# Performance work log

Hardware: AMD Instinct MI355X
Metric: run time of the kernel (lower is better)

The kernel has to match this reference:

```python
import jax, jax.numpy as jnp
import numpy as np

N = 4096       # num nodes
E = 131072     # num edges (avg degree 32)
IN = 256
HID = 512
OUT = 64


def _linear_params(k, fan_in, fan_out):
    kw, kb = jax.random.split(k)
    s = 1.0 / np.sqrt(fan_in)
    W = jax.random.uniform(kw, (fan_in, fan_out), jnp.float32, -s, s)
    b = jax.random.uniform(kb, (fan_out,), jnp.float32, -s, s)
    return W, b


def setup_inputs() -> dict:
    key = jax.random.key(0)
    ks = jax.random.split(key, 8)
    x = jax.random.normal(ks[0], (N, IN), jnp.float32)
    edge_index = jax.random.randint(ks[1], (2, E), 0, N, jnp.int32)
    ego_W, ego_b = _linear_params(ks[2], IN, HID)
    cut_W, cut_b = _linear_params(ks[3], IN, HID)
    glob_W, glob_b = _linear_params(ks[4], IN, HID)
    fc_W, fc_b = _linear_params(ks[5], 3 * HID, OUT)
    return dict(x=x, edge_index=edge_index, ego_W=ego_W, ego_b=ego_b,
                cut_W=cut_W, cut_b=cut_b, glob_W=glob_W, glob_b=glob_b,
                fc_W=fc_W, fc_b=fc_b)


def reference(x, edge_index, ego_W, ego_b, cut_W, cut_b, glob_W, glob_b, fc_W, fc_b):
    src, dst = edge_index[0], edge_index[1]
    n = x.shape[0]

    # --- extract_ego_subgraph: mean of x over the unique 2-hop in-neighborhood
    # (k_hop_subgraph flow='source_to_target': walk edges backward), incl. self.
    # B[t, s] = 1 iff edge s -> t exists.
    B = jnp.zeros((n, n), jnp.float32).at[dst, src].set(1.0)
    eye = jnp.eye(n, dtype=jnp.float32)
    reach = ((eye + B + B @ B) > 0).astype(jnp.float32)   # [N, N] bool-as-float
    ego_feat = (reach @ x) / reach.sum(axis=1, keepdims=True)  # counts >= 1 (self)

    # --- extract_cut_subgraph: drop a random half of the edges, then mean of
    # target features over kept out-edges per source node; fallback to x.
    perm = jax.random.permutation(jax.random.key(42), E)
    keep = jnp.ones(E, bool).at[perm[: E // 2]].set(False).astype(x.dtype)  # [E]
    sums = jax.ops.segment_sum(x[dst] * keep[:, None], src, num_segments=n)
    cnt = jax.ops.segment_sum(keep, src, num_segments=n)
    cut_feat = jnp.where((cnt > 0)[:, None], sums / jnp.maximum(cnt, 1.0)[:, None], x)

    # --- MessagePassingLayer: relu(scatter_add(linear(x)[src] -> dst))
    def mp(feat, W, b):
        h = feat @ W + b
        agg = jax.ops.segment_sum(h[src], dst, num_segments=n)
        return jax.nn.relu(agg)

    ego_enc = mp(ego_feat, ego_W, ego_b)
    cut_enc = mp(cut_feat, cut_W, cut_b)
    glob_enc = x @ glob_W + glob_b

    combined = jnp.concatenate([ego_enc, cut_enc, glob_enc], axis=-1)  # [N, 3H]
    out = combined @ fc_W + fc_b
    return jax.nn.log_softmax(out, axis=1)
```

## Files before the change

### kernel.cpp

```cpp
#include <hip/hip_runtime.h>

#define NN 4096
#define NE 131072
#define DIN 256
#define DHID 512
#define DOUT 64
#define DCAT 1536
#define NBINS 65536
#define HALF_E 65536

typedef __attribute__((ext_vector_type(8))) short short8;
typedef __attribute__((ext_vector_type(4))) float f32x4;

__device__ inline unsigned short bf16rne(float f){
  unsigned u = __float_as_uint(f);
  unsigned r = u + 0x7FFFu + ((u>>16)&1u);
  return (unsigned short)(r>>16);
}
__device__ inline float bf2f(unsigned short u){ return __uint_as_float(((unsigned)u)<<16); }

struct K2 { unsigned a, b; };
__host__ __device__ constexpr unsigned rotl32(unsigned x, unsigned d){ return (x<<d)|(x>>(32u-d)); }
__host__ __device__ constexpr K2 tf2x32(unsigned k0, unsigned k1, unsigned x0, unsigned x1){
  unsigned k2 = k0 ^ k1 ^ 0x1BD11BDAu;
  x0 += k0; x1 += k1;
  x0+=x1; x1=rotl32(x1,13); x1^=x0;
  x0+=x1; x1=rotl32(x1,15); x1^=x0;
  x0+=x1; x1=rotl32(x1,26); x1^=x0;
  x0+=x1; x1=rotl32(x1, 6); x1^=x0;
  x0+=k1; x1+=k2+1u;
  x0+=x1; x1=rotl32(x1,17); x1^=x0;
  x0+=x1; x1=rotl32(x1,29); x1^=x0;
  x0+=x1; x1=rotl32(x1,16); x1^=x0;
  x0+=x1; x1=rotl32(x1,24); x1^=x0;
  x0+=k2; x1+=k0+2u;
  x0+=x1; x1=rotl32(x1,13); x1^=x0;
  x0+=x1; x1=rotl32(x1,15); x1^=x0;
  x0+=x1; x1=rotl32(x1,26); x1^=x0;
  x0+=x1; x1=rotl32(x1, 6); x1^=x0;
  x0+=k0; x1+=k1+3u;
  x0+=x1; x1=rotl32(x1,17); x1^=x0;
  x0+=x1; x1=rotl32(x1,29); x1^=x0;
  x0+=x1; x1=rotl32(x1,16); x1^=x0;
  x0+=x1; x1=rotl32(x1,24); x1^=x0;
  x0+=k1; x1+=k2+4u;
  x0+=x1; x1=rotl32(x1,13); x1^=x0;
  x0+=x1; x1=rotl32(x1,15); x1^=x0;
  x0+=x1; x1=rotl32(x1,26); x1^=x0;
  x0+=x1; x1=rotl32(x1, 6); x1^=x0;
  x0+=k2; x1+=k0+5u;
  return K2{x0,x1};
}
static_assert(tf2x32(0u,0u,0u,2u).a==4146024105u, "threefry mismatch o0");
static_assert(tf2x32(0u,0u,0u,2u).b==2718843009u, "threefry mismatch o1");
static_assert(tf2x32(0u,0u,1u,3u).a==967050713u,  "threefry mismatch o0b");
static_assert(tf2x32(0u,0u,1u,3u).b==1272950319u, "threefry mismatch o1b");

constexpr K2 E0 = tf2x32(0u,42u,0u,0u);
constexpr K2 E1 = tf2x32(0u,42u,0u,1u);
constexpr unsigned SK1A = E1.a, SK1B = E1.b;
constexpr K2 F1 = tf2x32(E0.a,E0.b,0u,1u);
constexpr unsigned SK2A = F1.a, SK2B = F1.b;

#define MED_CAP 64

__device__ inline void tconv(const float* __restrict__ src, unsigned short* __restrict__ dst,
                             int R, int C, int r0, int c0){
  __shared__ unsigned short tile[64][72];
  int t = threadIdx.x;
  int tr = t>>2, tc = (t&3)*16;
  #pragma unroll
  for (int u=0;u<16;u++)
    tile[tr][tc+u] = bf16rne(src[(size_t)(r0+tr)*C + c0 + tc + u]);
  __syncthreads();
  unsigned short v[16];
  #pragma unroll
  for (int u=0;u<16;u++) v[u] = tile[tc+u][tr];
  uint4* vv = (uint4*)v;
  uint4* o = (uint4*)&dst[(size_t)(c0+tr)*R + r0 + tc];
  o[0] = vv[0]; o[1] = vv[1];
}

__global__ void front_k(const int* __restrict__ ei,
                        unsigned* __restrict__ keys1, unsigned* __restrict__ keys2,
                        unsigned* __restrict__ hist1, unsigned* __restrict__ hist2,
                        unsigned* __restrict__ indeg, unsigned* __restrict__ outdeg,
                        unsigned* __restrict__ bits,
                        const float* __restrict__ x, unsigned short* __restrict__ x_bf,
                        unsigned short* __restrict__ xT_bf,
                        const float* __restrict__ W0, unsigned short* __restrict__ WT0,
                        const float* __restrict__ W1, unsigned short* __restrict__ WT1,
                        const float* __restrict__ W2, unsigned short* __restrict__ WT2,
                        const float* __restrict__ fcW, unsigned short* __restrict__ fcWT){
  int b = blockIdx.x, t = threadIdx.x;
  if (b < 512){
    unsigned e = b*256u + t;
    K2 r1 = tf2x32(SK1A, SK1B, 0u, e);
    unsigned k1 = r1.a ^ r1.b;
    K2 r2 = tf2x32(SK2A, SK2B, 0u, e);
    unsigned k2 = r2.a ^ r2.b;
    keys1[e] = k1; keys2[e] = k2;
    atomicAdd(&hist1[k1>>16], 1u);
    atomicAdd(&hist2[k2>>16], 1u);
    unsigned s = (unsigned)ei[e], d = (unsigned)ei[NE+e];
    atomicAdd(&outdeg[s], 1u);
    atomicAdd(&indeg[d], 1u);
    atomicOr(&bits[d*128 + (s>>5)], 1u << (s&31));
    if (e < NN) atomicOr(&bits[e*128 + (e>>5)], 1u << (e&31));
    return;
  }
  int b2 = b - 512;
  if (b2 < 256){
    __shared__ unsigned short tile[64][72];
    int r0 = (b2>>2)*64, c0 = (b2&3)*64;
    int tr = t>>2, tc = (t&3)*16;
    #pragma unroll
    for (int u=0;u<16;u++)
      tile[tr][tc+u] = bf16rne(x[(size_t)(r0+tr)*DIN + c0 + tc + u]);
    __syncthreads();
    unsigned short vr[16];
    #pragma unroll
    for (int u=0;u<16;u++) vr[u] = tile[tr][tc+u];
    uint4* rv = (uint4*)vr;
    uint4* xo = (uint4*)&x_bf[(size_t)(r0+tr)*DIN + c0 + tc];
    xo[0] = rv[0]; xo[1] = rv[1];
    unsigned short v[16];
    #pragma unroll
    for (int u=0;u<16;u++) v[u] = tile[tc+u][tr];
    uint4* vv = (uint4*)v;
    uint4* o = (uint4*)&xT_bf[(size_t)(c0+tr)*NN + r0 + tc];
    o[0] = vv[0]; o[1] = vv[1];
  } else if (b2 < 352){
    int idx = b2 - 256;
    int z = idx >> 5, tl = idx & 31;
    const float* src = z==0?W0 : z==1?W1 : W2;
    unsigned short* dst = z==0?WT0 : z==1?WT1 : WT2;
    tconv(src, dst, DIN, DHID, (tl>>3)*64, (tl&7)*64);
  } else {
    int by = b2 - 352;
    tconv(fcW, fcWT, DCAT, DOUT, by*64, 0);
  }
}

__global__ void scanAll_k(const unsigned* __restrict__ in0, const unsigned* __restrict__ in1,
                          const unsigned* __restrict__ in2, const unsigned* __restrict__ in3,
                          unsigned* __restrict__ o0, unsigned* __restrict__ o1,
                          unsigned* __restrict__ o2, unsigned* __restrict__ o3,
                          unsigned* __restrict__ c0, unsigned* __restrict__ c1,
                          unsigned* __restrict__ c2, unsigned* __restrict__ c3,
                          unsigned* __restrict__ flags, const unsigned* __restrict__ hist2,
                          unsigned* __restrict__ med){
  int y = blockIdx.y;
  int nblk = (y<2) ? (NBINS/256) : (NN/256);
  int xb = blockIdx.x;
  if (xb >= nblk) return;
  const unsigned* in = y==0?in0 : y==1?in1 : y==2?in2 : in3;
  unsigned* o        = y==0?o0  : y==1?o1  : y==2?o2  : o3;
  unsigned* c        = y==0?c0  : y==1?c1  : y==2?c2  : c3;
  __shared__ unsigned s[256];
  __shared__ unsigned base_s;
  int t = threadIdx.x; unsigned i = xb*256u + t;
  unsigned v = in[i]; s[t] = v; __syncthreads();
  for (int off=1; off<256; off<<=1){
    unsigned u = (t>=off)?s[t-off]:0u; __syncthreads();
    s[t]+=u; __syncthreads();
  }
  unsigned excl = s[t]-v;
  unsigned total = s[255];
  unsigned* f = flags + y*256;
  if (xb == 0){
    if (t==0){ atomicExch(&f[0], 0x80000000u | total); base_s = 0u; }
  } else {
    if (t==0) atomicExch(&f[xb], 0x40000000u | total);
    if (t < 64){
      unsigned base = 0; int start = xb-1; int done = 0;
      while (!done && start >= 0){
        int idx = start - t;
        unsigned fv = 0;
        if (idx >= 0){
          do { fv = atomicAdd(&f[idx], 0u); } while (!(fv & 0xC0000000u));
        }
        unsigned long long pm = __ballot(idx >= 0 && (fv & 0x80000000u));
        unsigned contrib;
        if (pm){
          int plane = __ffsll((long long)pm) - 1;
          contrib = (idx >= 0 && t <= plane) ? (fv & 0x3FFFFFFFu) : 0u;
          done = 1;
        } else {
          contrib = (idx >= 0) ? (fv & 0x3FFFFFFFu) : 0u;
          start -= 64;
        }
        for (int oo=32; oo>0; oo>>=1) contrib += __shfl_xor(contrib, oo, 64);
        base += contrib;
      }
      if (t==0){ atomicExch(&f[xb], 0x80000000u | (base + total)); base_s = base; }
    }
  }
  __syncthreads();
  unsigned res = excl + base_s;
  o[i] = res; c[i] = res;
  if (y==1){
    unsigned hv = hist2[i];
    if (res <= HALF_E && HALF_E < res + hv){ med[0] = i; med[1] = res; }
  }
}

__global__ void scat1med_k(const unsigned* __restrict__ keys1, const unsigned* __restrict__ keys2,
                           unsigned* __restrict__ cursor, unsigned long long* __restrict__ slowstb,
                           unsigned* __restrict__ med){
  int e = blockIdx.x*256 + threadIdx.x;
  unsigned k = keys1[e];
  unsigned p = atomicAdd(&cursor[k>>16], 1u);
  slowstb[p] = ((unsigned long long)(k & 0xFFFFu) << 32) | (unsigned)e;
  unsigned k2 = keys2[e];
  if ((k2>>16) == med[0]){
    unsigned idx = atomicAdd(&med[2], 1u);
    if (idx < MED_CAP){ med[8+idx] = k2 & 0xFFFFu; med[72+idx] = (unsigned)e; }
  }
}

__global__ void rankscat_k(const int* __restrict__ ei, const unsigned* __restrict__ keys1,
                           const unsigned* __restrict__ prefix, const unsigned* __restrict__ hist,
                           const unsigned long long* __restrict__ slowstb,
                           unsigned* __restrict__ curin, unsigned* __restrict__ curout,
                           unsigned* __restrict__ in_list, unsigned* __restrict__ out_list,
                           unsigned* __restrict__ med){
  int b = blockIdx.x, t = threadIdx.x;
  if (b == NE/256){
    unsigned n = med[2]; if (n > MED_CAP) n = MED_CAP;
    unsigned qcut = HALF_E - med[1];
    if (t < (int)n){
      unsigned lo = med[8+t], rk = med[72+t], pos = 0;
      for (unsigned j=0;j<n;j++){
        unsigned lj = med[8+j], rj = med[72+j];
        if (lj < lo || (lj==lo && rj < rk)) pos++;
      }
      if (pos == qcut){ med[3] = lo; med[4] = rk; }
    }
    return;
  }
  int e = b*256 + t;
  unsigned k = keys1[e], h = k>>16;
  unsigned long long me = ((unsigned long long)(k & 0xFFFFu) << 32) | (unsigned)e;
  unsigned base = prefix[h], n = hist[h], r = 0;
  for (unsigned j=0;j<n;j++)
    r += (slowstb[base+j] < me) ? 1u : 0u;
  unsigned rk = base + r;
  unsigned s = (unsigned)ei[e], d = (unsigned)ei[NE+e];
  unsigned p = atomicAdd(&curin[d], 1u);  in_list[p] = s;
  unsigned q = atomicAdd(&curout[s], 1u); out_list[q] = d | (rk<<12);
}

__global__ void reachcut_k(const unsigned* __restrict__ bits, const unsigned* __restrict__ in_off,
                           const unsigned* __restrict__ in_list, const unsigned* __restrict__ indeg,
                           unsigned* __restrict__ reach, float* __restrict__ cntinv,
                           const float* __restrict__ x, const unsigned* __restrict__ out_off,
                           const unsigned* __restrict__ outdeg, const unsigned* __restrict__ out_list,
                           const unsigned* __restrict__ keys2, const unsigned* __restrict__ med,
                           unsigned short* __restrict__ cut_bf){
  __shared__ unsigned nbr[256];
  int b = blockIdx.x, t = threadIdx.x;
  if (b < NN){
    __shared__ int ws4[4];
    int i = b;
    unsigned off = in_off[i], deg = indeg[i];
    unsigned acc = (t < 128) ? bits[i*128 + t] : 0u;
    for (unsigned base=0; base<deg; base+=256){
      unsigned ch = min(deg-base, 256u);
      if (t < (int)ch) nbr[t] = in_list[off+base+t];
      __syncthreads();
      if (t < 128){
        #pragma unroll 4
        for (unsigned j=0;j<ch;j++) acc |= bits[nbr[j]*128 + t];
      }
      __syncthreads();
    }
    if (t < 128) reach[i*128 + t] = acc;
    int c = __popc(acc);
    for (int o=32;o>0;o>>=1) c += __shfl_xor(c, o, 64);
    if ((t&63)==0) ws4[t>>6] = c;
    __syncthreads();
    if (t==0) cntinv[i] = 1.0f / (float)(ws4[0]+ws4[1]+ws4[2]+ws4[3]);
  } else {
    __shared__ unsigned key_s[256];
    int s = b - NN;
    unsigned off = out_off[s], deg = outdeg[s];
    unsigned hs = med[0], loc = med[3], rkc = med[4];
    float acc = 0.f; int cnt = 0;
    for (unsigned base=0; base<deg; base+=256){
      unsigned ch = min(deg-base, 256u);
      if (t < (int)ch){
        unsigned v = out_list[off+base+t];
        nbr[t] = v;
        key_s[t] = keys2[v >> 12];
      }
      __syncthreads();
      #pragma unroll 4
      for (unsigned j=0;j<ch;j++){
        unsigned v = nbr[j], k2 = key_s[j];
        unsigned rk = v >> 12;
        unsigned h = k2>>16, lo = k2 & 0xFFFFu;
        unsigned keep = (h > hs) || (h == hs && (lo > loc || (lo == loc && rk >= rkc)));
        if (keep){ cnt++; acc += x[(size_t)(v & 0xFFFu)*DIN + t]; }
      }
      __syncthreads();
    }
    float v = cnt ? acc / (float)cnt : x[(size_t)s*DIN + t];
    cut_bf[(size_t)s*DIN + t] = bf16rne(v);
  }
}

__global__ void bitgemm_k(const unsigned* __restrict__ reach, const unsigned short* __restrict__ xT,
                          float* __restrict__ pbuf){
  __shared__ __align__(16) unsigned short bt[4][64*32];
  int t = threadIdx.x, w = t>>6, l = t&63;
  int m0 = blockIdx.x*64, n0 = blockIdx.y*64;
  int kbase = blockIdx.z*(NN/4);
  int srow = t>>2, sg = t&3;
  int arow = m0 + 16*w + (l&15);
  int lg = l>>4;
  f32x4 acc[4];
  #pragma unroll
  for (int c=0;c<4;c++) acc[c] = f32x4{0.f,0.f,0.f,0.f};

  for (int it=0; it<8; ++it){
    int kk = kbase + it*128;
    __syncthreads();
    #pragma unroll
    for (int s=0;s<4;s++){
      uint4 v = *(const uint4*)&xT[(size_t)(n0+srow)*NN + kk + 32*s + sg*8];
      *(uint4*)&bt[s][srow*32 + ((sg ^ (srow&3))*8)] = v;
    }
    __syncthreads();
    unsigned rw[4];
    *(uint4*)rw = *(const uint4*)&reach[(size_t)arow*128 + (kk>>5)];
    #pragma unroll
    for (int s=0;s<4;s++){
      unsigned byte = (rw[s] >> (8*lg)) & 0xFFu;
      union { short8 s8; unsigned u[4]; } af;
      #pragma unroll
      for (int pp=0;pp<4;pp++){
        unsigned b0 = (byte>>(2*pp))&1u, b1 = (byte>>(2*pp+1))&1u;
        af.u[pp] = b0*0x3F80u | b1*0x3F800000u;
      }
      #pragma unroll
      for (int c=0;c<4;c++){
        int brow = 16*c + (l&15);
        short8 bf = *(const short8*)&bt[s][brow*32 + ((lg ^ (brow&3))*8)];
        acc[c] = __builtin_amdgcn_mfma_f32_16x16x32_bf16(af.s8, bf, acc[c], 0,0,0);
      }
    }
  }
  size_t zoff = (size_t)blockIdx.z*NN*DIN;
  #pragma unroll
  for (int c=0;c<4;c++){
    #pragma unroll
    for (int r=0;r<4;r++){
      int row = m0 + 16*w + 4*lg + r;
      int col = n0 + 16*c + (l&15);
      pbuf[zoff + (size_t)row*DIN + col] = acc[c][r];
    }
  }
}

__global__ void redscale_k(const float* __restrict__ pbuf, const float* __restrict__ cntinv,
                           unsigned short* __restrict__ ego_bf){
  int g = blockIdx.x*256 + threadIdx.x;
  const size_t S = (size_t)NN*DIN/4;
  const float4* p4 = (const float4*)pbuf;
  float4 a = p4[g], b = p4[g+S], c = p4[g+2*S], d = p4[g+3*S];
  int row = (g*4)>>8;
  float ci = cntinv[row];
  float vx = (a.x+b.x+c.x+d.x)*ci, vy = (a.y+b.y+c.y+d.y)*ci;
  float vz = (a.z+b.z+c.z+d.z)*ci, vw = (a.w+b.w+c.w+d.w)*ci;
  uint2 o;
  o.x = (unsigned)bf16rne(vx) | ((unsigned)bf16rne(vy)<<16);
  o.y = (unsigned)bf16rne(vz) | ((unsigned)bf16rne(vw)<<16);
  ((uint2*)ego_bf)[g] = o;
}

__global__ void aggfeat_k(const unsigned short* __restrict__ ego_bf, const unsigned short* __restrict__ cut_bf,
                          const unsigned* __restrict__ in_off, const unsigned* __restrict__ indeg,
                          const unsigned* __restrict__ in_list,
                          unsigned short* __restrict__ aggE, unsigned short* __restrict__ aggC){
  __shared__ unsigned nbr[256];
  int i = blockIdx.x, t = threadIdx.x;
  unsigned off = in_off[i], deg = indeg[i];
  float ae = 0.f, ac = 0.f;
  for (unsigned base=0; base<deg; base+=256){
    unsigned ch = min(deg-base, 256u);
    if (t < (int)ch) nbr[t] = in_list[off+base+t];
    __syncthreads();
    #pragma unroll 4
    for (unsigned j=0;j<ch;j++){
      unsigned s = nbr[j];
      ae += bf2f(ego_bf[(size_t)s*DIN + t]);
      ac += bf2f(cut_bf[(size_t)s*DIN + t]);
    }
    __syncthreads();
  }
  aggE[(size_t)i*DIN + t] = bf16rne(ae);
  aggC[(size_t)i*DIN + t] = bf16rne(ac);
}

__global__ void gemm3_k(const unsigned short* __restrict__ aggE, const unsigned short* __restrict__ aggC,
                        const unsigned short* __restrict__ xbf,
                        const unsigned short* __restrict__ WTe, const unsigned short* __restrict__ WTc,
                        const unsigned short* __restrict__ WTg,
                        const float* __restrict__ eb, const float* __restrict__ cb, const float* __restrict__ gb,
                        const unsigned* __restrict__ indeg, unsigned short* __restrict__ hcat){
  __shared__ __align__(16) unsigned short at[4][64*32];
  __shared__ __align__(16) unsigned short bt[4][64*32];
  int z = blockIdx.z;
  const unsigned short* A  = z==0? aggE : z==1? aggC : xbf;
  const unsigned short* BT = z==0? WTe  : z==1? WTc  : WTg;
  const float* bias        = z==0? eb   : z==1? cb   : gb;
  int t = threadIdx.x, w = t>>6, l = t&63;
  int n0 = blockIdx.x*64, m0 = blockIdx.y*64;
  int srow = t>>2, sg = t&3;
  int lg = l>>4;
  f32x4 acc[4];
  #pragma unroll
  for (int c=0;c<4;c++) acc[c] = f32x4{0.f,0.f,0.f,0.f};

  for (int it=0; it<2; ++it){
    int kk = it*128;
    __syncthreads();
    #pragma unroll
    for (int s=0;s<4;s++){
      uint4 va = *(const uint4*)&A [(size_t)(m0+srow)*DIN + kk + 32*s + sg*8];
      uint4 vb = *(const uint4*)&BT[(size_t)(n0+srow)*DIN + kk + 32*s + sg*8];
      *(uint4*)&at[s][srow*32 + ((sg ^ (srow&3))*8)] = va;
      *(uint4*)&bt[s][srow*32 + ((sg ^ (srow&3))*8)] = vb;
    }
    __syncthreads();
    int ar = 16*w + (l&15);
    #pragma unroll
    for (int s=0;s<4;s++){
      short8 af = *(const short8*)&at[s][ar*32 + ((lg ^ (ar&3))*8)];
      #pragma unroll
      for (int c=0;c<4;c++){
        int brow = 16*c + (l&15);
        short8 bf = *(const short8*)&bt[s][brow*32 + ((lg ^ (brow&3))*8)];
        acc[c] = __builtin_amdgcn_mfma_f32_16x16x32_bf16(af, bf, acc[c], 0,0,0);
      }
    }
  }
  #pragma unroll
  for (int c=0;c<4;c++){
    #pragma unroll
    for (int r=0;r<4;r++){
      int row = m0 + 16*w + 4*lg + r;
      int col = n0 + 16*c + (l&15);
      float scale = (z<2) ? (float)indeg[row] : 1.0f;
      float v = acc[c][r] + bias[col]*scale;
      if (z<2) v = fmaxf(v, 0.f);
      hcat[(size_t)row*DCAT + z*DHID + col] = bf16rne(v);
    }
  }
}

__global__ void fcsm_k(const unsigned short* __restrict__ hcat, const unsigned short* __restrict__ fcWT,
                       const float* __restrict__ fcb, float* __restrict__ out){
  __shared__ __align__(16) unsigned short at[4][64*32];
  __shared__ __align__(16) unsigned short bt[4][64*32];
  int t = threadIdx.x, w = t>>6, l = t&63;
  int m0 = blockIdx.x*64;
  int srow = t>>2, sg = t&3;
  int lg = l>>4;
  f32x4 acc[4];
  #pragma unroll
  for (int c=0;c<4;c++) acc[c] = f32x4{0.f,0.f,0.f,0.f};

  for (int it=0; it<12; ++it){
    int kk = it*128;
    __syncthreads();
    #pragma unroll
    for (int s=0;s<4;s++){
      uint4 va = *(const uint4*)&hcat [(size_t)(m0+srow)*DCAT + kk + 32*s + sg*8];
      uint4 vb = *(const uint4*)&fcWT[(size_t)srow*DCAT + kk + 32*s + sg*8];
      *(uint4*)&at[s][srow*32 + ((sg ^ (srow&3))*8)] = va;
      *(uint4*)&bt[s][srow*32 + ((sg ^ (srow&3))*8)] = vb;
    }
    __syncthreads();
    int ar = 16*w + (l&15);
    #pragma unroll
    for (int s=0;s<4;s++){
      short8 af = *(const short8*)&at[s][ar*32 + ((lg ^ (ar&3))*8)];
      #pragma unroll
      for (int c=0;c<4;c++){
        int brow = 16*c + (l&15);
        short8 bf = *(const short8*)&bt[s][brow*32 + ((lg ^ (brow&3))*8)];
        acc[c] = __builtin_amdgcn_mfma_f32_16x16x32_bf16(af, bf, acc[c], 0,0,0);
      }
    }
  }
  #pragma unroll
  for (int r=0;r<4;r++){
    int row = m0 + 16*w + 4*lg + r;
    float v0 = acc[0][r] + fcb[(l&15)];
    float v1 = acc[1][r] + fcb[16 + (l&15)];
    float v2 = acc[2][r] + fcb[32 + (l&15)];
    float v3 = acc[3][r] + fcb[48 + (l&15)];
    float m = fmaxf(fmaxf(v0,v1), fmaxf(v2,v3));
    m = fmaxf(m, __shfl_xor(m, 1, 64));
    m = fmaxf(m, __shfl_xor(m, 2, 64));
    m = fmaxf(m, __shfl_xor(m, 4, 64));
    m = fmaxf(m, __shfl_xor(m, 8, 64));
    float s = __expf(v0-m) + __expf(v1-m) + __expf(v2-m) + __expf(v3-m);
    s += __shfl_xor(s, 1, 64);
    s += __shfl_xor(s, 2, 64);
    s += __shfl_xor(s, 4, 64);
    s += __shfl_xor(s, 8, 64);
    float ls = logf(s);
    size_t ro = (size_t)row*DOUT + (l&15);
    out[ro]      = (v0 - m) - ls;
    out[ro + 16] = (v1 - m) - ls;
    out[ro + 32] = (v2 - m) - ls;
    out[ro + 48] = (v3 - m) - ls;
  }
}

static inline size_t alignup(size_t x){ return (x + 255) & ~(size_t)255; }

extern "C" void kernel_launch(void* const* d_in, const int* in_sizes, int n_in,
                              void* d_out, int out_size, void* d_ws, size_t ws_size,
                              hipStream_t stream) {
  const float* x      = (const float*)d_in[0];
  const int*   ei     = (const int*)  d_in[1];
  const float* ego_W  = (const float*)d_in[2];
  const float* ego_b  = (const float*)d_in[3];
  const float* cut_W  = (const float*)d_in[4];
  const float* cut_b  = (const float*)d_in[5];
  const float* glob_W = (const float*)d_in[6];
  const float* glob_b = (const float*)d_in[7];
  const float* fc_W   = (const float*)d_in[8];
  const float* fc_b   = (const float*)d_in[9];
  float* out = (float*)d_out;

  char* base = (char*)d_ws;
  char* p = base;
  #define ALLOC(ty, name, cnt) ty* name = (ty*)p; p += alignup(sizeof(ty)*(size_t)(cnt));
  ALLOC(char,           R0,      (size_t)4*NN*DIN*4);
  ALLOC(unsigned,       bits,    NN*128);
  ALLOC(unsigned,       indeg,   NN);
  ALLOC(unsigned,       outdeg,  NN);
  ALLOC(unsigned,       hist1,   NBINS);
  ALLOC(unsigned,       hist2,   NBINS);
  ALLOC(unsigned,       med,     256);
  ALLOC(unsigned,       flags,   1024);
  char* zero_end = p;
  ALLOC(unsigned,       in_off,  NN);
  ALLOC(unsigned,       out_off, NN);
  ALLOC(unsigned,       curin,   NN);
  ALLOC(unsigned,       curout,  NN);
  ALLOC(unsigned,       in_list, NE);
  ALLOC(unsigned,       out_list,NE);
  ALLOC(unsigned,       reach,   NN*128);
  ALLOC(float,          cntinv,  NN);
  ALLOC(unsigned short, x_bf,    (size_t)NN*DIN);
  ALLOC(unsigned short, xT_bf,   (size_t)DIN*NN);
  ALLOC(unsigned short, ego_bf,  (size_t)NN*DIN);
  ALLOC(unsigned short, cut_bf,  (size_t)NN*DIN);
  ALLOC(unsigned short, aggE_bf, (size_t)NN*DIN);
  ALLOC(unsigned short, aggC_bf, (size_t)NN*DIN);
  ALLOC(unsigned short, egoWT,   (size_t)DHID*DIN);
  ALLOC(unsigned short, cutWT,   (size_t)DHID*DIN);
  ALLOC(unsigned short, globWT,  (size_t)DHID*DIN);
  ALLOC(unsigned short, fcWT,    (size_t)DOUT*DCAT);
  ALLOC(unsigned,       prefix1, NBINS);
  ALLOC(unsigned,       cursor1, NBINS);
  ALLOC(unsigned,       prefix2, NBINS);
  ALLOC(unsigned,       cursor2, NBINS);
  #undef ALLOC
  size_t need = (size_t)(p - base);
  if (ws_size < need){
    hipMemsetAsync(d_out, 0x7F, (size_t)out_size*sizeof(float), stream);
    return;
  }
  float*          pbuf = (float*)R0;
  unsigned short* hcat = (unsigned short*)R0;
  char* q = R0;
  #define OALLOC(ty, name, cnt) ty* name = (ty*)q; q += alignup(sizeof(ty)*(size_t)(cnt));
  OALLOC(unsigned,            keys1,   NE);
  OALLOC(unsigned,            keys2,   NE);
  OALLOC(unsigned long long,  slowstb, NE);
  #undef OALLOC

  const int EB = NE/256;

  hipMemsetAsync(bits, 0, (size_t)(zero_end - (char*)bits), stream);
  hipLaunchKernelGGL(front_k, dim3(888), dim3(256), 0, stream,
                     ei, keys1, keys2, hist1, hist2, indeg, outdeg, bits,
                     x, x_bf, xT_bf, ego_W, egoWT, cut_W, cutWT, glob_W, globWT, fc_W, fcWT);
  hipLaunchKernelGGL(scanAll_k, dim3(NBINS/256, 4), dim3(256), 0, stream,
                     hist1, hist2, indeg, outdeg,
                     prefix1, prefix2, in_off, out_off,
                     cursor1, cursor2, curin, curout, flags, hist2, med);
  hipLaunchKernelGGL(scat1med_k, dim3(EB), dim3(256), 0, stream,
                     keys1, keys2, cursor1, slowstb, med);
  hipLaunchKernelGGL(rankscat_k, dim3(EB+1), dim3(256), 0, stream,
                     ei, keys1, prefix1, hist1, slowstb, curin, curout, in_list, out_list, med);
  hipLaunchKernelGGL(reachcut_k, dim3(2*NN), dim3(256), 0, stream,
                     bits, in_off, in_list, indeg, reach, cntinv,
                     x, out_off, outdeg, out_list, keys2, med, cut_bf);
  hipLaunchKernelGGL(bitgemm_k, dim3(NN/64, DIN/64, 4), dim3(256), 0, stream, reach, xT_bf, pbuf);
  hipLaunchKernelGGL(redscale_k, dim3((NN*DIN/4)/256), dim3(256), 0, stream, pbuf, cntinv, ego_bf);
  hipLaunchKernelGGL(aggfeat_k, dim3(NN), dim3(256), 0, stream,
                     ego_bf, cut_bf, in_off, indeg, in_list, aggE_bf, aggC_bf);
  hipLaunchKernelGGL(gemm3_k, dim3(DHID/64, NN/64, 3), dim3(256), 0, stream,
                     aggE_bf, aggC_bf, x_bf, egoWT, cutWT, globWT,
                     ego_b, cut_b, glob_b, indeg, hcat);
  hipLaunchKernelGGL(fcsm_k, dim3(NN/64), dim3(256), 0, stream, hcat, fcWT, fc_b, out);
}
```

Baseline: 175.2 us.

## Split neighbor gathers across wavefronts with vector loads; pad GEMM LDS tiles

The reach, cut-feature and aggregation kernels now spread neighbors across the four wavefronts, each handling every fourth neighbor. Each lane loads several elements per neighbor as uint2 or float4, and the partial sums are combined through shared memory at the end. Before, only some threads were active and each issued scalar loads, so the goal is more memory-level parallelism and wider loads. Separately, the GEMM LDS tiles drop the XOR swizzle in favour of a padded row stride of 40 to avoid bank conflicts, at the cost of extra LDS and a final reduction step.

```diff
diff --git a/kernel.cpp b/kernel.cpp
--- a/kernel.cpp
+++ b/kernel.cpp
@@ -64,6 +64,8 @@
 
 #define MED_CAP 64
 
+#define LDW 40
+
 __device__ inline void tconv(const float* __restrict__ src, unsigned short* __restrict__ dst,
                              int R, int C, int r0, int c0){
   __shared__ unsigned short tile[64][72];
@@ -260,33 +262,42 @@
                            unsigned short* __restrict__ cut_bf){
   __shared__ unsigned nbr[256];
   int b = blockIdx.x, t = threadIdx.x;
+  int g = t>>6, l = t&63;
   if (b < NN){
-    __shared__ int ws4[4];
+    __shared__ unsigned combA[4][64], combB[4][64];
     int i = b;
     unsigned off = in_off[i], deg = indeg[i];
-    unsigned acc = (t < 128) ? bits[i*128 + t] : 0u;
+    unsigned a0=0u, a1=0u;
+    if (g==0){ uint2 sb = *(const uint2*)&bits[(size_t)i*128 + l*2]; a0=sb.x; a1=sb.y; }
     for (unsigned base=0; base<deg; base+=256){
       unsigned ch = min(deg-base, 256u);
       if (t < (int)ch) nbr[t] = in_list[off+base+t];
       __syncthreads();
-      if (t < 128){
-        #pragma unroll 4
-        for (unsigned j=0;j<ch;j++) acc |= bits[nbr[j]*128 + t];
+      for (unsigned j=g; j<ch; j+=4){
+        uint2 v = *(const uint2*)&bits[(size_t)nbr[j]*128 + l*2];
+        a0 |= v.x; a1 |= v.y;
       }
       __syncthreads();
     }
-    if (t < 128) reach[i*128 + t] = acc;
-    int c = __popc(acc);
-    for (int o=32;o>0;o>>=1) c += __shfl_xor(c, o, 64);
-    if ((t&63)==0) ws4[t>>6] = c;
-    __syncthreads();
-    if (t==0) cntinv[i] = 1.0f / (float)(ws4[0]+ws4[1]+ws4[2]+ws4[3]);
+    combA[g][l]=a0; combB[g][l]=a1;
+    __syncthreads();
+    if (g==0){
+      a0 |= combA[1][l] | combA[2][l] | combA[3][l];
+      a1 |= combB[1][l] | combB[2][l] | combB[3][l];
+      uint2 o; o.x=a0; o.y=a1;
+      *(uint2*)&reach[(size_t)i*128 + l*2] = o;
+      int c = __popc(a0) + __popc(a1);
+      for (int oo=32;oo>0;oo>>=1) c += __shfl_xor(c, oo, 64);
+      if (l==0) cntinv[i] = 1.0f / (float)c;
+    }
   } else {
     __shared__ unsigned key_s[256];
+    __shared__ float4 combF[4][64];
+    __shared__ int combC[4];
     int s = b - NN;
     unsigned off = out_off[s], deg = outdeg[s];
     unsigned hs = med[0], loc = med[3], rkc = med[4];
-    float acc = 0.f; int cnt = 0;
+    float4 acc = {0.f,0.f,0.f,0.f}; int cnt = 0;
     for (unsigned base=0; base<deg; base+=256){
       unsigned ch = min(deg-base, 256u);
       if (t < (int)ch){
@@ -295,24 +306,41 @@
         key_s[t] = keys2[v >> 12];
       }
       __syncthreads();
-      #pragma unroll 4
-      for (unsigned j=0;j<ch;j++){
+      for (unsigned j=g; j<ch; j+=4){
         unsigned v = nbr[j], k2 = key_s[j];
         unsigned rk = v >> 12;
         unsigned h = k2>>16, lo = k2 & 0xFFFFu;
         unsigned keep = (h > hs) || (h == hs && (lo > loc || (lo == loc && rk >= rkc)));
-        if (keep){ cnt++; acc += x[(size_t)(v & 0xFFFu)*DIN + t]; }
+        if (keep){
+          cnt++;
+          float4 xv = *(const float4*)&x[(size_t)(v & 0xFFFu)*DIN + l*4];
+          acc.x += xv.x; acc.y += xv.y; acc.z += xv.z; acc.w += xv.w;
+        }
       }
       __syncthreads();
     }
-    float v = cnt ? acc / (float)cnt : x[(size_t)s*DIN + t];
-    cut_bf[(size_t)s*DIN + t] = bf16rne(v);
+    combF[g][l] = acc;
+    if (l==0) combC[g] = cnt;
+    __syncthreads();
+    if (g==0){
+      float4 a1 = combF[1][l], a2 = combF[2][l], a3 = combF[3][l];
+      float sx = acc.x+a1.x+a2.x+a3.x, sy = acc.y+a1.y+a2.y+a3.y;
+      float sz = acc.z+a1.z+a2.z+a3.z, sw = acc.w+a1.w+a2.w+a3.w;
+      int c = combC[0]+combC[1]+combC[2]+combC[3];
+      float vx, vy, vz, vw;
+      if (c){ float ci = 1.0f/(float)c; vx=sx*ci; vy=sy*ci; vz=sz*ci; vw=sw*ci; }
+      else { float4 xv = *(const float4*)&x[(size_t)s*DIN + l*4]; vx=xv.x; vy=xv.y; vz=xv.z; vw=xv.w; }
+      uint2 o;
+      o.x = (unsigned)bf16rne(vx) | ((unsigned)bf16rne(vy)<<16);
+      o.y = (unsigned)bf16rne(vz) | ((unsigned)bf16rne(vw)<<16);
+      *(uint2*)&cut_bf[(size_t)s*DIN + l*4] = o;
+    }
   }
 }
 
 __global__ void bitgemm_k(const unsigned* __restrict__ reach, const unsigned short* __restrict__ xT,
                           float* __restrict__ pbuf){
-  __shared__ __align__(16) unsigned short bt[4][64*32];
+  __shared__ __align__(16) unsigned short bt[4][64*LDW];
   int t = threadIdx.x, w = t>>6, l = t&63;
   int m0 = blockIdx.x*64, n0 = blockIdx.y*64;
   int kbase = blockIdx.z*(NN/4);
@@ -329,7 +357,7 @@
     #pragma unroll
     for (int s=0;s<4;s++){
       uint4 v = *(const uint4*)&xT[(size_t)(n0+srow)*NN + kk + 32*s + sg*8];
-      *(uint4*)&bt[s][srow*32 + ((sg ^ (srow&3))*8)] = v;
+      *(uint4*)&bt[s][srow*LDW + sg*8] = v;
     }
     __syncthreads();
     unsigned rw[4];
@@ -346,7 +374,7 @@
       #pragma unroll
       for (int c=0;c<4;c++){
         int brow = 16*c + (l&15);
-        short8 bf = *(const short8*)&bt[s][brow*32 + ((lg ^ (brow&3))*8)];
+        short8 bf = *(const short8*)&bt[s][brow*LDW + lg*8];
         acc[c] = __builtin_amdgcn_mfma_f32_16x16x32_bf16(af.s8, bf, acc[c], 0,0,0);
       }
     }
@@ -384,23 +412,47 @@
                           const unsigned* __restrict__ in_list,
                           unsigned short* __restrict__ aggE, unsigned short* __restrict__ aggC){
   __shared__ unsigned nbr[256];
+  __shared__ float4 combE[4][64], combD[4][64];
   int i = blockIdx.x, t = threadIdx.x;
+  int g = t>>6, l = t&63;
   unsigned off = in_off[i], deg = indeg[i];
-  float ae = 0.f, ac = 0.f;
+  float4 ae = {0.f,0.f,0.f,0.f}, ac = {0.f,0.f,0.f,0.f};
   for (unsigned base=0; base<deg; base+=256){
     unsigned ch = min(deg-base, 256u);
     if (t < (int)ch) nbr[t] = in_list[off+base+t];
     __syncthreads();
-    #pragma unroll 4
-    for (unsigned j=0;j<ch;j++){
+    for (unsigned j=g; j<ch; j+=4){
       unsigned s = nbr[j];
-      ae += bf2f(ego_bf[(size_t)s*DIN + t]);
-      ac += bf2f(cut_bf[(size_t)s*DIN + t]);
-    }
-    __syncthreads();
-  }
-  aggE[(size_t)i*DIN + t] = bf16rne(ae);
-  aggC[(size_t)i*DIN + t] = bf16rne(ac);
+      uint2 ev = *(const uint2*)&ego_bf[(size_t)s*DIN + l*4];
+      uint2 cv = *(const uint2*)&cut_bf[(size_t)s*DIN + l*4];
+      ae.x += bf2f((unsigned short)(ev.x & 0xFFFFu));
+      ae.y += bf2f((unsigned short)(ev.x >> 16));
+      ae.z += bf2f((unsigned short)(ev.y & 0xFFFFu));
+      ae.w += bf2f((unsigned short)(ev.y >> 16));
+      ac.x += bf2f((unsigned short)(cv.x & 0xFFFFu));
+      ac.y += bf2f((unsigned short)(cv.x >> 16));
+      ac.z += bf2f((unsigned short)(cv.y & 0xFFFFu));
+      ac.w += bf2f((unsigned short)(cv.y >> 16));
+    }
+    __syncthreads();
+  }
+  combE[g][l] = ae; combD[g][l] = ac;
+  __syncthreads();
+  if (g==0){
+    float4 e1 = combE[1][l], e2 = combE[2][l], e3 = combE[3][l];
+    float4 c1 = combD[1][l], c2 = combD[2][l], c3 = combD[3][l];
+    float ex = ae.x+e1.x+e2.x+e3.x, ey = ae.y+e1.y+e2.y+e3.y;
+    float ez = ae.z+e1.z+e2.z+e3.z, ew = ae.w+e1.w+e2.w+e3.w;
+    float cx = ac.x+c1.x+c2.x+c3.x, cy = ac.y+c1.y+c2.y+c3.y;
+    float cz = ac.z+c1.z+c2.z+c3.z, cw = ac.w+c1.w+c2.w+c3.w;
+    uint2 oe, oc;
+    oe.x = (unsigned)bf16rne(ex) | ((unsigned)bf16rne(ey)<<16);
+    oe.y = (unsigned)bf16rne(ez) | ((unsigned)bf16rne(ew)<<16);
+    oc.x = (unsigned)bf16rne(cx) | ((unsigned)bf16rne(cy)<<16);
+    oc.y = (unsigned)bf16rne(cz) | ((unsigned)bf16rne(cw)<<16);
+    *(uint2*)&aggE[(size_t)i*DIN + l*4] = oe;
+    *(uint2*)&aggC[(size_t)i*DIN + l*4] = oc;
+  }
 }
 
 __global__ void gemm3_k(const unsigned short* __restrict__ aggE, const unsigned short* __restrict__ aggC,
@@ -409,8 +461,8 @@
                         const unsigned short* __restrict__ WTg,
                         const float* __restrict__ eb, const float* __restrict__ cb, const float* __restrict__ gb,
                         const unsigned* __restrict__ indeg, unsigned short* __restrict__ hcat){
-  __shared__ __align__(16) unsigned short at[4][64*32];
-  __shared__ __align__(16) unsigned short bt[4][64*32];
+  __shared__ __align__(16) unsigned short at[4][64*LDW];
+  __shared__ __align__(16) unsigned short bt[4][64*LDW];
   int z = blockIdx.z;
   const unsigned short* A  = z==0? aggE : z==1? aggC : xbf;
   const unsigned short* BT = z==0? WTe  : z==1? WTc  : WTg;
@@ -430,18 +482,18 @@
     for (int s=0;s<4;s++){
       uint4 va = *(const uint4*)&A [(size_t)(m0+srow)*DIN + kk + 32*s + sg*8];
       uint4 vb = *(const uint4*)&BT[(size_t)(n0+srow)*DIN + kk + 32*s + sg*8];
-      *(uint4*)&at[s][srow*32 + ((sg ^ (srow&3))*8)] = va;
-      *(uint4*)&bt[s][srow*32 + ((sg ^ (srow&3))*8)] = vb;
+      *(uint4*)&at[s][srow*LDW + sg*8] = va;
+      *(uint4*)&bt[s][srow*LDW + sg*8] = vb;
     }
     __syncthreads();
     int ar = 16*w + (l&15);
     #pragma unroll
     for (int s=0;s<4;s++){
-      short8 af = *(const short8*)&at[s][ar*32 + ((lg ^ (ar&3))*8)];
+      short8 af = *(const short8*)&at[s][ar*LDW + lg*8];
       #pragma unroll
       for (int c=0;c<4;c++){
         int brow = 16*c + (l&15);
-        short8 bf = *(const short8*)&bt[s][brow*32 + ((lg ^ (brow&3))*8)];
+        short8 bf = *(const short8*)&bt[s][brow*LDW + lg*8];
         acc[c] = __builtin_amdgcn_mfma_f32_16x16x32_bf16(af, bf, acc[c], 0,0,0);
       }
     }
@@ -462,8 +514,8 @@
 
 __global__ void fcsm_k(const unsigned short* __restrict__ hcat, const unsigned short* __restrict__ fcWT,
                        const float* __restrict__ fcb, float* __restrict__ out){
-  __shared__ __align__(16) unsigned short at[4][64*32];
-  __shared__ __align__(16) unsigned short bt[4][64*32];
+  __shared__ __align__(16) unsigned short at[4][64*LDW];
+  __shared__ __align__(16) unsigned short bt[4][64*LDW];
   int t = threadIdx.x, w = t>>6, l = t&63;
   int m0 = blockIdx.x*64;
   int srow = t>>2, sg = t&3;
@@ -479,18 +531,18 @@
     for (int s=0;s<4;s++){
       uint4 va = *(const uint4*)&hcat [(size_t)(m0+srow)*DCAT + kk + 32*s + sg*8];
       uint4 vb = *(const uint4*)&fcWT[(size_t)srow*DCAT + kk + 32*s + sg*8];
-      *(uint4*)&at[s][srow*32 + ((sg ^ (srow&3))*8)] = va;
-      *(uint4*)&bt[s][srow*32 + ((sg ^ (srow&3))*8)] = vb;
+      *(uint4*)&at[s][srow*LDW + sg*8] = va;
+      *(uint4*)&bt[s][srow*LDW + sg*8] = vb;
     }
     __syncthreads();
     int ar = 16*w + (l&15);
     #pragma unroll
     for (int s=0;s<4;s++){
-      short8 af = *(const short8*)&at[s][ar*32 + ((lg ^ (ar&3))*8)];
+      short8 af = *(const short8*)&at[s][ar*LDW + lg*8];
       #pragma unroll
       for (int c=0;c<4;c++){
         int brow = 16*c + (l&15);
-        short8 bf = *(const short8*)&bt[s][brow*32 + ((lg ^ (brow&3))*8)];
+        short8 bf = *(const short8*)&bt[s][brow*LDW + lg*8];
         acc[c] = __builtin_amdgcn_mfma_f32_16x16x32_bf16(af, bf, acc[c], 0,0,0);
       }
     }
```

Result: faster. 165.9 us (-5.3%).
